# Performance work log

Measured on AMD Instinct MI355X. Metric: run time of the kernel, lower is better.

## Reference

```python
import jax, jax.numpy as jnp
import numpy as np

EPS = 1e-6
H = 12  # num_attention_heads

def _phi(x):
    # feature map used by fast-transformers LinearAttention: elu(x) + 1
    return jax.nn.elu(x) + 1.0

def setup_inputs() -> dict:
    key = jax.random.key(0)
    k1, k2, k3 = jax.random.split(key, 3)
    B, N, D = 32, 1024, 768
    x = jax.random.normal(k1, (B, N, D), dtype=jnp.float32)
    W_qkv = jax.random.normal(k2, (D, 3 * D), dtype=jnp.float32) * (D ** -0.5)
    W_out = jax.random.normal(k3, (D, D), dtype=jnp.float32) * (D ** -0.5)
    b_out = jnp.zeros((D,), dtype=jnp.float32)
    return {"x": x, "W_qkv": W_qkv, "W_out": W_out, "b_out": b_out}

def reference(x, W_qkv, W_out, b_out):
    B, N, D = x.shape
    d = D // H
    # F.pad(x, [0,0,0,1]): append one zero token along sequence
    x_ = jnp.pad(x, ((0, 0), (0, 1), (0, 0)))              # [B, N+1, D]
    qkv = x_ @ W_qkv                                        # [B, N+1, 3D]
    q, k, v = jnp.split(qkv, 3, axis=-1)
    q = q.reshape(B, N + 1, H, d)
    k = k.reshape(B, N + 1, H, d)
    v = v.reshape(B, N + 1, H, d)
    # non-causal linear attention (mask is all-ones -> no masking)
    q = _phi(q)
    k = _phi(k)
    kv = jnp.einsum('bshd,bshm->bhdm', k, v)                # [B, H, d, d]
    z = 1.0 / (jnp.einsum('blhd,bhd->blh', q, k.sum(axis=1)) + EPS)
    out = jnp.einsum('blhd,bhdm,blh->blhm', q, kv, z)       # [B, N+1, H, d]
    out = out.reshape(B, N + 1, D)
    out = out @ W_out + b_out                               # dropout = identity (eval)
    return out[:, :-1, :]                                   # drop padding token
```

## Files before the change

### kernel.cpp

```cpp
#include <hip/hip_runtime.h>
#include <hip/hip_bf16.h>


typedef __bf16 bf16x8 __attribute__((ext_vector_type(8)));
typedef float f32x4 __attribute__((ext_vector_type(4)));

__device__ __forceinline__ ushort f2bf(float f) {
  union { float f; unsigned u; } x; x.f = f;
  unsigned r = x.u + 0x7fffu + ((x.u >> 16) & 1u);
  return (ushort)(r >> 16);
}
__device__ __forceinline__ float bf2f(ushort h) {
  union { unsigned u; float f; } x; x.u = ((unsigned)h) << 16;
  return x.f;
}
__device__ __forceinline__ void gload_lds16(const void* g, void* lds) {
  __builtin_amdgcn_global_load_lds((const __attribute__((address_space(1))) void*)g,
                                   (__attribute__((address_space(3))) void*)lds, 16, 0, 0);
}

__global__ __launch_bounds__(256) void cvt_f32_bf16(const float* __restrict__ in,
                                                    ushort* __restrict__ out, int n4) {
  int i = blockIdx.x * 256 + threadIdx.x;
  if (i >= n4) return;
  float4 v = reinterpret_cast<const float4*>(in)[i];
  ushort4 o;
  o.x = f2bf(v.x); o.y = f2bf(v.y); o.z = f2bf(v.z); o.w = f2bf(v.w);
  reinterpret_cast<ushort4*>(out)[i] = o;
}

__global__ __launch_bounds__(256) void transpose_cvt(const float* __restrict__ src,
                                                     ushort* __restrict__ dst, int R, int C) {
  __shared__ float tile[32][33];
  int bc = blockIdx.x * 32, br = blockIdx.y * 32;
  int tx = threadIdx.x & 31, ty = threadIdx.x >> 5;
  #pragma unroll
  for (int i = 0; i < 32; i += 8)
    tile[ty + i][tx] = src[(size_t)(br + ty + i) * C + (bc + tx)];
  __syncthreads();
  #pragma unroll
  for (int i = 0; i < 32; i += 8)
    dst[(size_t)(bc + ty + i) * R + (br + tx)] = f2bf(tile[tx][ty + i]);
}

template <int MODE>
__global__ __launch_bounds__(512, 2) void gemm256(const ushort* __restrict__ A,
                                                  const ushort* __restrict__ Bt,
                                                  void* __restrict__ C,
                                                  const float* __restrict__ bias,
                                                  int N, int K, int nbx, int cpx) {
  extern __shared__ ushort lds[];
  const int tid = threadIdx.x;
  const int lane = tid & 63;
  const int wid = tid >> 6;
  const int wm = wid >> 2, wn = wid & 3;
  const int laneR = lane & 15, laneS = lane >> 4;

  const int bid = blockIdx.x;
  const int lin = (bid & 7) * cpx + (bid >> 3);
  const int by = lin / nbx, bx = lin - by * nbx;
  const int m0 = by * 256, n0 = bx * 256;
  const int NT = K >> 6;

  const int sr = tid >> 2, ss = tid & 3;
  const int sslot = ss ^ ((tid >> 3) & 3);
  const ushort* Asrc0 = A + (size_t)(m0 + sr) * K + sslot * 8;
  const ushort* Bsrc0 = Bt + (size_t)(n0 + sr) * K + sslot * 8;
  const size_t rowstep = (size_t)128 * K;
  const int ldst0 = tid * 8;

  const int sprime = laneS ^ ((laneR >> 1) & 3);
  const int aoff = (wm * 128 + laneR) * 32 + sprime * 8;
  const int boff = 16384 + (wn * 64 + laneR) * 32 + sprime * 8;

  f32x4 acc[8][4] = {};

  #pragma unroll
  for (int ks = 0; ks < 2; ++ks)
    #pragma unroll
    for (int i = 0; i < 2; ++i) {
      gload_lds16(Asrc0 + ks * 32 + (size_t)i * rowstep, lds + ks * 8192 + i * 4096 + ldst0);
      gload_lds16(Bsrc0 + ks * 32 + (size_t)i * rowstep, lds + 16384 + ks * 8192 + i * 4096 + ldst0);
    }
  asm volatile("s_waitcnt vmcnt(0)" ::: "memory");
  __builtin_amdgcn_s_barrier();
  asm volatile("" ::: "memory");

  for (int t = 0; t < NT; ++t) {
    const int cur = t & 1;
    const ushort* __restrict__ buf = lds + cur * 32768;
    ushort* __restrict__ nbuf = lds + (cur ^ 1) * 32768;
    const int kt1 = (t + 1) << 6;
    const bool pre = (t + 1 < NT);
    bf16x8 bfr[4], afr[4];
    #pragma unroll
    for (int ks = 0; ks < 2; ++ks) {
      #pragma unroll
      for (int rh = 0; rh < 2; ++rh) {
        if (rh == 0) {
          #pragma unroll
          for (int j = 0; j < 4; ++j)
            bfr[j] = *(const bf16x8*)(buf + ks * 8192 + boff + j * 512);
        }
        #pragma unroll
        for (int ii = 0; ii < 4; ++ii)
          afr[ii] = *(const bf16x8*)(buf + ks * 8192 + aoff + (rh * 4 + ii) * 512);
        if (rh == 0 && pre) {
          #pragma unroll
          for (int i = 0; i < 2; ++i) {
            gload_lds16(Asrc0 + kt1 + ks * 32 + (size_t)i * rowstep,
                        nbuf + ks * 8192 + i * 4096 + ldst0);
            gload_lds16(Bsrc0 + kt1 + ks * 32 + (size_t)i * rowstep,
                        nbuf + 16384 + ks * 8192 + i * 4096 + ldst0);
          }
        }
        if (rh == 1) {
          if (ks == 0) {
            if (pre) asm volatile("s_waitcnt vmcnt(4)" ::: "memory");
            else     asm volatile("s_waitcnt vmcnt(0)" ::: "memory");
          } else if (pre) {
            asm volatile("s_waitcnt vmcnt(4)" ::: "memory");
          }
        }
        __builtin_amdgcn_sched_barrier(0);
        __builtin_amdgcn_s_barrier();
        asm volatile("" ::: "memory");
        __builtin_amdgcn_sched_barrier(0);
        __builtin_amdgcn_s_setprio(1);
        #pragma unroll
        for (int ii = 0; ii < 4; ++ii)
          #pragma unroll
          for (int j = 0; j < 4; ++j)
            acc[rh * 4 + ii][j] =
                __builtin_amdgcn_mfma_f32_16x16x32_bf16(afr[ii], bfr[j], acc[rh * 4 + ii][j], 0, 0, 0);
        __builtin_amdgcn_s_setprio(0);
        __builtin_amdgcn_sched_barrier(0);
        asm volatile("" ::: "memory");
        __builtin_amdgcn_s_barrier();
      }
    }
  }

  #pragma unroll
  for (int i = 0; i < 8; ++i) {
    const int grow0 = m0 + wm * 128 + i * 16 + (laneS << 2);
    #pragma unroll
    for (int j = 0; j < 4; ++j) {
      const int gcol = n0 + wn * 64 + j * 16 + laneR;
      #pragma unroll
      for (int r = 0; r < 4; ++r) {
        float v = acc[i][j][r];
        if (MODE == 0) {
          if (gcol < 1536) v = (v > 0.f) ? (v + 1.f) : __expf(v);
          reinterpret_cast<ushort*>(C)[(size_t)(grow0 + r) * N + gcol] = f2bf(v);
        } else {
          reinterpret_cast<float*>(C)[(size_t)(grow0 + r) * N + gcol] = v + bias[gcol];
        }
      }
    }
  }
}

__global__ __launch_bounds__(256) void kv_partial(const ushort* __restrict__ qkv,
                                                  float* __restrict__ kv_part,
                                                  float* __restrict__ ks_part) {
  const int blk = blockIdx.x;
  const int bh = blk >> 2, sp = blk & 3;
  const int b = bh / 12, h = bh % 12;
  const int tid = threadIdx.x;
  __shared__ ushort Ks[32 * 64];
  __shared__ ushort Vs[32 * 64];
  float acc[4][4] = {};
  float kacc[4] = {};
  const int dq0 = (tid & 15) * 4, mq0 = (tid >> 4) * 4;
  const int r = tid >> 3, o = tid & 7;
  for (int st = 0; st < 256; st += 32) {
    const int s0 = sp * 256 + st;
    __syncthreads();
    const size_t rowbase = (size_t)(b * 1024 + s0 + r) * 2304 + h * 64 + o * 8;
    gload_lds16(qkv + rowbase + 768,  &Ks[tid * 8]);
    gload_lds16(qkv + rowbase + 1536, &Vs[tid * 8]);
    asm volatile("s_waitcnt vmcnt(0)" ::: "memory");
    __syncthreads();
    #pragma unroll 8
    for (int s = 0; s < 32; ++s) {
      short4 kk = *reinterpret_cast<const short4*>(&Ks[s * 64 + dq0]);
      short4 vv = *reinterpret_cast<const short4*>(&Vs[s * 64 + mq0]);
      float kf[4] = { bf2f((ushort)kk.x), bf2f((ushort)kk.y), bf2f((ushort)kk.z), bf2f((ushort)kk.w) };
      float vf[4] = { bf2f((ushort)vv.x), bf2f((ushort)vv.y), bf2f((ushort)vv.z), bf2f((ushort)vv.w) };
      #pragma unroll
      for (int jm = 0; jm < 4; ++jm)
        #pragma unroll
        for (int id = 0; id < 4; ++id)
          acc[jm][id] += vf[jm] * kf[id];
      if (mq0 == 0) {
        #pragma unroll
        for (int id = 0; id < 4; ++id) kacc[id] += kf[id];
      }
    }
  }
  float* kvp = kv_part + ((size_t)sp * 384 + bh) * 4096;
  #pragma unroll
  for (int jm = 0; jm < 4; ++jm)
    #pragma unroll
    for (int id = 0; id < 4; ++id)
      kvp[(mq0 + jm) * 64 + dq0 + id] = acc[jm][id];
  if (mq0 == 0) {
    #pragma unroll
    for (int id = 0; id < 4; ++id)
      ks_part[((size_t)sp * 384 + bh) * 64 + dq0 + id] = kacc[id];
  }
}

__global__ __launch_bounds__(256) void kv_reduce(const float* __restrict__ kv_part,
                                                 const float* __restrict__ ks_part,
                                                 ushort* __restrict__ kv_bf,
                                                 float* __restrict__ ksum) {
  int i = blockIdx.x * 256 + threadIdx.x;
  if (i < 384 * 4096) {
    float s = 0.f;
    #pragma unroll
    for (int p = 0; p < 4; ++p) s += kv_part[(size_t)p * (384 * 4096) + i];
    kv_bf[i] = f2bf(s);
  }
  if (i < 384 * 64) {
    float s = 1.0f;
    #pragma unroll
    for (int p = 0; p < 4; ++p) s += ks_part[(size_t)p * (384 * 64) + i];
    ksum[i] = s;
  }
}

__global__ __launch_bounds__(256) void attn_kernel(const ushort* __restrict__ qkv,
                                                   const ushort* __restrict__ kv_bf,
                                                   const float* __restrict__ ksum,
                                                   ushort* __restrict__ attn) {
  const int blk = blockIdx.x;
  const int bh = blk >> 3, tb = blk & 7;
  const int b = bh / 12, h = bh % 12;
  const int row0 = b * 1024 + tb * 128;
  __shared__ ushort Qs[128 * 64];
  __shared__ ushort KVs[64 * 64];
  __shared__ float zs[128];
  __shared__ float ks_lds[64];
  const int tid = threadIdx.x;
  const int lane = tid & 63, w = tid >> 6;
  #pragma unroll
  for (int j = 0; j < 4; ++j) {
    int c = j * 256 + tid;
    gload_lds16(qkv + (size_t)(row0 + (c >> 3)) * 2304 + h * 64 + (c & 7) * 8, &Qs[c * 8]);
  }
  #pragma unroll
  for (int j = 0; j < 2; ++j) {
    int c = j * 256 + tid;
    gload_lds16(kv_bf + (size_t)bh * 4096 + c * 8, &KVs[c * 8]);
  }
  if (tid < 64) ks_lds[tid] = ksum[bh * 64 + tid];
  asm volatile("s_waitcnt vmcnt(0)" ::: "memory");
  __syncthreads();
  if (tid < 128) {
    float d = 0.f;
    #pragma unroll 8
    for (int e = 0; e < 64; ++e) d += bf2f(Qs[tid * 64 + e]) * ks_lds[e];
    zs[tid] = 1.f / (d + 1e-6f);
  }
  __syncthreads();
  f32x4 acc[2][4] = {};
  #pragma unroll
  for (int ks = 0; ks < 2; ++ks) {
    bf16x8 a[2], bb[4];
    #pragma unroll
    for (int i = 0; i < 2; ++i)
      a[i] = *reinterpret_cast<const bf16x8*>(&Qs[(w * 32 + i * 16 + (lane & 15)) * 64 + ks * 32 + (lane >> 4) * 8]);
    #pragma unroll
    for (int j = 0; j < 4; ++j)
      bb[j] = *reinterpret_cast<const bf16x8*>(&KVs[(j * 16 + (lane & 15)) * 64 + ks * 32 + (lane >> 4) * 8]);
    #pragma unroll
    for (int i = 0; i < 2; ++i)
      #pragma unroll
      for (int j = 0; j < 4; ++j)
        acc[i][j] = __builtin_amdgcn_mfma_f32_16x16x32_bf16(a[i], bb[j], acc[i][j], 0, 0, 0);
  }
  #pragma unroll
  for (int i = 0; i < 2; ++i) {
    const int t0 = w * 32 + i * 16 + ((lane >> 4) << 2);
    #pragma unroll
    for (int j = 0; j < 4; ++j) {
      const int m = j * 16 + (lane & 15);
      #pragma unroll
      for (int r = 0; r < 4; ++r) {
        float v = acc[i][j][r] * zs[t0 + r];
        attn[(size_t)(row0 + t0 + r) * 768 + h * 64 + m] = f2bf(v);
      }
    }
  }
}

extern "C" void kernel_launch(void* const* d_in, const int* in_sizes, int n_in,
                              void* d_out, int out_size, void* d_ws, size_t ws_size,
                              hipStream_t stream) {
  (void)in_sizes; (void)n_in; (void)out_size; (void)ws_size;
  const float* x    = (const float*)d_in[0];
  const float* Wqkv = (const float*)d_in[1];
  const float* Wout = (const float*)d_in[2];
  const float* bout = (const float*)d_in[3];
  float* out = (float*)d_out;
  char* ws = (char*)d_ws;

  ushort* xbf    = (ushort*)(ws);
  ushort* wqkvT  = (ushort*)(ws + 50331648);
  ushort* woutT  = (ushort*)(ws + 53870592);
  ushort* qkv    = (ushort*)(ws + 55050240);
  float*  ksp    = (float*) (ws + 206045184);
  ushort* kvbf   = (ushort*)(ws + 206438400);
  float*  ksum   = (float*) (ws + 209584128);
  float*  kvpart = (float*)(ws);
  ushort* attn   = (ushort*)(ws);

  static const int LDS_BYTES = 131072;
  hipFuncSetAttribute(reinterpret_cast<const void*>(&gemm256<0>),
                      hipFuncAttributeMaxDynamicSharedMemorySize, LDS_BYTES);
  hipFuncSetAttribute(reinterpret_cast<const void*>(&gemm256<1>),
                      hipFuncAttributeMaxDynamicSharedMemorySize, LDS_BYTES);

  cvt_f32_bf16<<<24576, 256, 0, stream>>>(x, xbf, 6291456);
  transpose_cvt<<<dim3(72, 24), 256, 0, stream>>>(Wqkv, wqkvT, 768, 2304);
  transpose_cvt<<<dim3(24, 24), 256, 0, stream>>>(Wout, woutT, 768, 768);
  gemm256<0><<<1152, 512, LDS_BYTES, stream>>>(xbf, wqkvT, qkv, nullptr, 2304, 768, 9, 144);
  kv_partial<<<1536, 256, 0, stream>>>(qkv, kvpart, ksp);
  kv_reduce<<<6144, 256, 0, stream>>>(kvpart, ksp, kvbf, ksum);
  attn_kernel<<<3072, 256, 0, stream>>>(qkv, kvbf, ksum, attn);
  gemm256<1><<<384, 512, LDS_BYTES, stream>>>(attn, woutT, out, bout, 768, 768, 3, 48);
}
```

Measured before the change: 318.6 us.

## Restructure GEMM main loop into half-tile staged prefetch with deeper lookahead

Rewrites the bf16 MFMA GEMM main loop so global-to-LDS loads are issued in half-tile chunks spread across the four compute phases. The lookahead grows from one K tile to about one and a half, and the vmcnt waits become finer-grained. It also changes the LDS swizzle slot computation to use the row index. This aims to hide global load latency better and cut stalls at barriers. In exchange it adds more in-flight loads and more complex buffer reuse, where a subtle overwrite or ordering bug could corrupt data.

```diff
diff --git a/kernel.cpp b/kernel.cpp
--- a/kernel.cpp
+++ b/kernel.cpp
@@ -63,7 +63,7 @@
   const int NT = K >> 6;
 
   const int sr = tid >> 2, ss = tid & 3;
-  const int sslot = ss ^ ((tid >> 3) & 3);
+  const int sslot = ss ^ ((sr >> 1) & 3);
   const ushort* Asrc0 = A + (size_t)(m0 + sr) * K + sslot * 8;
   const ushort* Bsrc0 = Bt + (size_t)(n0 + sr) * K + sslot * 8;
   const size_t rowstep = (size_t)128 * K;
@@ -75,71 +75,108 @@
 
   f32x4 acc[8][4] = {};
 
-  #pragma unroll
-  for (int ks = 0; ks < 2; ++ks)
-    #pragma unroll
-    for (int i = 0; i < 2; ++i) {
-      gload_lds16(Asrc0 + ks * 32 + (size_t)i * rowstep, lds + ks * 8192 + i * 4096 + ldst0);
-      gload_lds16(Bsrc0 + ks * 32 + (size_t)i * rowstep, lds + 16384 + ks * 8192 + i * 4096 + ldst0);
-    }
+  #define STAGE_HT(SRC, KT, KS, DST)                                              \
+    { gload_lds16((SRC) + (KT) * 64 + (KS) * 32,                                  \
+                  (DST) + (KS) * 8192 + ldst0);                                   \
+      gload_lds16((SRC) + (KT) * 64 + (KS) * 32 + rowstep,                        \
+                  (DST) + (KS) * 8192 + 4096 + ldst0); }
+
+  {
+    ushort* b0 = lds;
+    ushort* b1 = lds + 32768;
+    STAGE_HT(Asrc0, 0, 0, b0);
+    STAGE_HT(Bsrc0, 0, 0, b0 + 16384);
+    STAGE_HT(Asrc0, 0, 1, b0);
+    STAGE_HT(Bsrc0, 0, 1, b0 + 16384);
+    STAGE_HT(Asrc0, 1, 0, b1);
+    STAGE_HT(Bsrc0, 1, 0, b1 + 16384);
+  }
+  asm volatile("s_waitcnt vmcnt(8)" ::: "memory");
+  __builtin_amdgcn_sched_barrier(0);
+  __builtin_amdgcn_s_barrier();
+  __builtin_amdgcn_sched_barrier(0);
+
+  for (int t = 0; t < NT; ++t) {
+    ushort* cbuf = lds + (t & 1) * 32768;
+    ushort* nbuf = lds + ((t & 1) ^ 1) * 32768;
+    const int t1 = (t + 1 < NT) ? t + 1 : t;
+    const int t2 = (t + 2 < NT) ? t + 2 : t;
+    bf16x8 afr[4], bfr[4];
+
+    #pragma unroll
+    for (int j = 0; j < 4; ++j)
+      bfr[j] = *(const bf16x8*)(cbuf + boff + j * 512);
+    #pragma unroll
+    for (int ii = 0; ii < 4; ++ii)
+      afr[ii] = *(const bf16x8*)(cbuf + aoff + ii * 512);
+    STAGE_HT(Asrc0, t1, 1, nbuf);
+    __builtin_amdgcn_sched_barrier(0);
+    __builtin_amdgcn_s_barrier();
+    __builtin_amdgcn_s_setprio(1);
+    #pragma unroll
+    for (int ii = 0; ii < 4; ++ii)
+      #pragma unroll
+      for (int j = 0; j < 4; ++j)
+        acc[ii][j] = __builtin_amdgcn_mfma_f32_16x16x32_bf16(afr[ii], bfr[j], acc[ii][j], 0, 0, 0);
+    __builtin_amdgcn_s_setprio(0);
+    __builtin_amdgcn_s_barrier();
+    __builtin_amdgcn_sched_barrier(0);
+
+    #pragma unroll
+    for (int ii = 0; ii < 4; ++ii)
+      afr[ii] = *(const bf16x8*)(cbuf + aoff + (4 + ii) * 512);
+    STAGE_HT(Bsrc0, t1, 1, nbuf + 16384);
+    asm volatile("s_waitcnt vmcnt(8)" ::: "memory");
+    __builtin_amdgcn_sched_barrier(0);
+    __builtin_amdgcn_s_barrier();
+    __builtin_amdgcn_s_setprio(1);
+    #pragma unroll
+    for (int ii = 0; ii < 4; ++ii)
+      #pragma unroll
+      for (int j = 0; j < 4; ++j)
+        acc[4 + ii][j] = __builtin_amdgcn_mfma_f32_16x16x32_bf16(afr[ii], bfr[j], acc[4 + ii][j], 0, 0, 0);
+    __builtin_amdgcn_s_setprio(0);
+    __builtin_amdgcn_s_barrier();
+    __builtin_amdgcn_sched_barrier(0);
+
+    #pragma unroll
+    for (int j = 0; j < 4; ++j)
+      bfr[j] = *(const bf16x8*)(cbuf + 8192 + boff + j * 512);
+    #pragma unroll
+    for (int ii = 0; ii < 4; ++ii)
+      afr[ii] = *(const bf16x8*)(cbuf + 8192 + aoff + ii * 512);
+    STAGE_HT(Asrc0, t2, 0, cbuf);
+    __builtin_amdgcn_sched_barrier(0);
+    __builtin_amdgcn_s_barrier();
+    __builtin_amdgcn_s_setprio(1);
+    #pragma unroll
+    for (int ii = 0; ii < 4; ++ii)
+      #pragma unroll
+      for (int j = 0; j < 4; ++j)
+        acc[ii][j] = __builtin_amdgcn_mfma_f32_16x16x32_bf16(afr[ii], bfr[j], acc[ii][j], 0, 0, 0);
+    __builtin_amdgcn_s_setprio(0);
+    __builtin_amdgcn_s_barrier();
+    __builtin_amdgcn_sched_barrier(0);
+
+    #pragma unroll
+    for (int ii = 0; ii < 4; ++ii)
+      afr[ii] = *(const bf16x8*)(cbuf + 8192 + aoff + (4 + ii) * 512);
+    STAGE_HT(Bsrc0, t2, 0, cbuf + 16384);
+    asm volatile("s_waitcnt vmcnt(8)" ::: "memory");
+    __builtin_amdgcn_sched_barrier(0);
+    __builtin_amdgcn_s_barrier();
+    __builtin_amdgcn_s_setprio(1);
+    #pragma unroll
+    for (int ii = 0; ii < 4; ++ii)
+      #pragma unroll
+      for (int j = 0; j < 4; ++j)
+        acc[4 + ii][j] = __builtin_amdgcn_mfma_f32_16x16x32_bf16(afr[ii], bfr[j], acc[4 + ii][j], 0, 0, 0);
+    __builtin_amdgcn_s_setprio(0);
+    __builtin_amdgcn_s_barrier();
+    __builtin_amdgcn_sched_barrier(0);
+  }
+  #undef STAGE_HT
   asm volatile("s_waitcnt vmcnt(0)" ::: "memory");
-  __builtin_amdgcn_s_barrier();
-  asm volatile("" ::: "memory");
-
-  for (int t = 0; t < NT; ++t) {
-    const int cur = t & 1;
-    const ushort* __restrict__ buf = lds + cur * 32768;
-    ushort* __restrict__ nbuf = lds + (cur ^ 1) * 32768;
-    const int kt1 = (t + 1) << 6;
-    const bool pre = (t + 1 < NT);
-    bf16x8 bfr[4], afr[4];
-    #pragma unroll
-    for (int ks = 0; ks < 2; ++ks) {
-      #pragma unroll
-      for (int rh = 0; rh < 2; ++rh) {
-        if (rh == 0) {
-          #pragma unroll
-          for (int j = 0; j < 4; ++j)
-            bfr[j] = *(const bf16x8*)(buf + ks * 8192 + boff + j * 512);
-        }
-        #pragma unroll
-        for (int ii = 0; ii < 4; ++ii)
-          afr[ii] = *(const bf16x8*)(buf + ks * 8192 + aoff + (rh * 4 + ii) * 512);
-        if (rh == 0 && pre) {
-          #pragma unroll
-          for (int i = 0; i < 2; ++i) {
-            gload_lds16(Asrc0 + kt1 + ks * 32 + (size_t)i * rowstep,
-                        nbuf + ks * 8192 + i * 4096 + ldst0);
-            gload_lds16(Bsrc0 + kt1 + ks * 32 + (size_t)i * rowstep,
-                        nbuf + 16384 + ks * 8192 + i * 4096 + ldst0);
-          }
-        }
-        if (rh == 1) {
-          if (ks == 0) {
-            if (pre) asm volatile("s_waitcnt vmcnt(4)" ::: "memory");
-            else     asm volatile("s_waitcnt vmcnt(0)" ::: "memory");
-          } else if (pre) {
-            asm volatile("s_waitcnt vmcnt(4)" ::: "memory");
-          }
-        }
-        __builtin_amdgcn_sched_barrier(0);
-        __builtin_amdgcn_s_barrier();
-        asm volatile("" ::: "memory");
-        __builtin_amdgcn_sched_barrier(0);
-        __builtin_amdgcn_s_setprio(1);
-        #pragma unroll
-        for (int ii = 0; ii < 4; ++ii)
-          #pragma unroll
-          for (int j = 0; j < 4; ++j)
-            acc[rh * 4 + ii][j] =
-                __builtin_amdgcn_mfma_f32_16x16x32_bf16(afr[ii], bfr[j], acc[rh * 4 + ii][j], 0, 0, 0);
-        __builtin_amdgcn_s_setprio(0);
-        __builtin_amdgcn_sched_barrier(0);
-        asm volatile("" ::: "memory");
-        __builtin_amdgcn_s_barrier();
-      }
-    }
-  }
 
   #pragma unroll
   for (int i = 0; i < 8; ++i) {
```

New measurement: 316.8 us. About the same (-0.6%).
